# Kernel tuning notes

Hardware: AMD Instinct MI355X
Metric: run time of the kernel (lower is better)

Reference implementation:

```python
import jax, jax.numpy as jnp
import numpy as np

N = 100000   # nodes
E = 600000   # edges
D = 128      # d_model / hidden_dim
L = 4        # num_layers
V = 5000     # node vocab (in_size)
G = 128      # num graphs in batch
C = 10       # num_class
BN_EPS = 1e-5


def setup_inputs() -> dict:
    key = jax.random.key(0)
    ks = jax.random.split(key, 20)
    s = 0.05
    return {
        "x": jax.random.randint(ks[0], (N,), 0, V),
        "edge_index": jax.random.randint(ks[1], (2, E), 0, N),
        "edge_attr": jax.random.normal(ks[2], (E, 2), dtype=jnp.float32),
        "batch": jnp.sort(jax.random.randint(ks[3], (N,), 0, G)),
        # embedding table
        "emb": jax.random.normal(ks[4], (V, D), dtype=jnp.float32) * s,
        # per-layer GINEConv edge linear (edge_dim=2 -> D)
        "edge_w": jax.random.normal(ks[5], (L, 2, D), dtype=jnp.float32) * s,
        "edge_b": jnp.zeros((L, D), jnp.float32),
        # per-layer MLP: Linear -> BN -> ReLU -> Linear
        "w1": jax.random.normal(ks[6], (L, D, D), dtype=jnp.float32) * s,
        "b1": jnp.zeros((L, D), jnp.float32),
        "g1": jnp.ones((L, D), jnp.float32),
        "beta1": jnp.zeros((L, D), jnp.float32),
        "w2": jax.random.normal(ks[7], (L, D, D), dtype=jnp.float32) * s,
        "b2": jnp.zeros((L, D), jnp.float32),
        # per-layer outer BatchNorm (self.norms)
        "ng": jnp.ones((L, D), jnp.float32),
        "nb": jnp.zeros((L, D), jnp.float32),
        # classifier: Linear(D,D) -> ReLU -> Linear(D,C)
        "cw1": jax.random.normal(ks[8], (D, D), dtype=jnp.float32) * s,
        "cb1": jnp.zeros((D,), jnp.float32),
        "cw2": jax.random.normal(ks[9], (D, C), dtype=jnp.float32) * s,
        "cb2": jnp.zeros((C,), jnp.float32),
    }


def _bn(h, g, b):
    # training-mode BatchNorm1d over node axis, biased variance
    m = h.mean(0)
    v = h.var(0)
    return (h - m) * jax.lax.rsqrt(v + BN_EPS) * g + b


def reference(x, edge_index, edge_attr, batch, emb, edge_w, edge_b,
              w1, b1, g1, beta1, w2, b2, ng, nb, cw1, cb1, cw2, cb2):
    h = emb[x]                                    # [N, D]
    src, dst = edge_index[0], edge_index[1]
    for l in range(L):
        e = edge_attr @ edge_w[l] + edge_b[l]     # [E, D]
        msg = jax.nn.relu(h[src] + e)             # gather + add + relu
        agg = jax.ops.segment_sum(msg, dst, num_segments=N)  # scatter-sum
        z = h + agg                               # (1+eps)*x_i + aggr, eps=0
        z = jax.nn.relu(_bn(z @ w1[l] + b1[l], g1[l], beta1[l]))
        h = _bn(z @ w2[l] + b2[l], ng[l], nb[l])
        if l != L - 1:
            h = jax.nn.relu(h)
    sums = jax.ops.segment_sum(h, batch, num_segments=G)            # [G, D]
    counts = jax.ops.segment_sum(jnp.ones((N, 1), h.dtype), batch, num_segments=G)
    pooled = sums / jnp.maximum(counts, 1.0)      # global mean pool
    return jax.nn.relu(pooled @ cw1 + cb1) @ cw2 + cb2  # [G, C]
```

## Files before the change

kernel.cpp:

```cpp
#include <hip/hip_runtime.h>
#include <stdint.h>

#define N_NODES 100000
#define N_EDGES 600000
#define DMODEL  128
#define NLAYERS 4
#define NGRAPH  128
#define NCLASS  10
#define BN_EPS  1e-5f
#define NSLOT   32
#define STATSZ  (NSLOT * 2 * DMODEL)

typedef __bf16 bf16x8 __attribute__((ext_vector_type(8)));
typedef __bf16 bf16x4 __attribute__((ext_vector_type(4)));
typedef __bf16 bf16x2 __attribute__((ext_vector_type(2)));
typedef float  f32x4  __attribute__((ext_vector_type(4)));

__global__ void k_init(int* __restrict__ deg, float* __restrict__ statA,
                       float* __restrict__ statB, float* __restrict__ psum,
                       const float* __restrict__ w1, const float* __restrict__ w2,
                       __bf16* __restrict__ wt_hi, __bf16* __restrict__ wt_lo,
                       const int* __restrict__ batch, int* __restrict__ gstart) {
  int i = blockIdx.x * 256 + threadIdx.x;
  if (i < N_NODES) deg[i] = 0;
  if (i < NLAYERS * STATSZ) {
    statA[i] = 0.0f;
    statB[i] = 0.0f;
  }
  if (i < NGRAPH * DMODEL) psum[i] = 0.0f;
  {
    int mat = i >> 14;
    int rem = i & 16383;
    int n = rem >> 7;
    int k = rem & 127;
    int l = mat >> 1;
    int which = mat & 1;
    const float* w = which ? w2 : w1;
    float v = w[(size_t)l * DMODEL * DMODEL + (size_t)k * DMODEL + n];
    __bf16 hi = (__bf16)v;
    wt_hi[i] = hi;
    wt_lo[i] = (__bf16)(v - (float)hi);
  }
  if (i <= NGRAPH) {
    int lo = 0;
    int hi = N_NODES;
    while (lo < hi) {
      int mid = (lo + hi) >> 1;
      if (batch[mid] < i) lo = mid + 1; else hi = mid;
    }
    gstart[i] = lo;
  }
}

__global__ void k_embed(const int* __restrict__ x, const float* __restrict__ emb,
                        __bf16* __restrict__ h) {
  int idx = blockIdx.x * 256 + threadIdx.x;
  if (idx >= N_NODES * DMODEL / 8) return;
  int i = idx >> 4;
  int p = idx & 15;
  const float* src = emb + (size_t)x[i] * DMODEL + p * 8;
  float4 v0 = *(const float4*)(src);
  float4 v1 = *(const float4*)(src + 4);
  bf16x8 o;
  o[0] = (__bf16)v0.x; o[1] = (__bf16)v0.y; o[2] = (__bf16)v0.z; o[3] = (__bf16)v0.w;
  o[4] = (__bf16)v1.x; o[5] = (__bf16)v1.y; o[6] = (__bf16)v1.z; o[7] = (__bf16)v1.w;
  *(bf16x8*)(h + (size_t)i * DMODEL + p * 8) = o;
}

__global__ void k_hist(const int* __restrict__ dst, int* __restrict__ deg) {
  int e = blockIdx.x * 256 + threadIdx.x;
  if (e < N_EDGES) atomicAdd(&deg[dst[e]], 1);
}

__global__ void k_scan1(const int* __restrict__ deg, int* __restrict__ out,
                        int* __restrict__ bsum, int n) {
  __shared__ int lds[256];
  int t = threadIdx.x;
  int idx = blockIdx.x * 256 + t;
  int v = (idx < n) ? deg[idx] : 0;
  int val = v;
  lds[t] = val;
  for (int ofs = 1; ofs < 256; ofs <<= 1) {
    __syncthreads();
    int u = (t >= ofs) ? lds[t - ofs] : 0;
    __syncthreads();
    val += u;
    lds[t] = val;
  }
  if (idx < n) out[idx] = val - v;
  if (t == 255) bsum[blockIdx.x] = val;
}

__global__ void k_scan2(const int* __restrict__ bsum, int* __restrict__ bsumx, int nb) {
  __shared__ int lds[512];
  int t = threadIdx.x;
  int v = (t < nb) ? bsum[t] : 0;
  int val = v;
  lds[t] = val;
  for (int ofs = 1; ofs < 512; ofs <<= 1) {
    __syncthreads();
    int u = (t >= ofs) ? lds[t - ofs] : 0;
    __syncthreads();
    val += u;
    lds[t] = val;
  }
  if (t < nb) bsumx[t] = val - v;
}

__global__ void k_scan3(int* __restrict__ row_start, int* __restrict__ cursor,
                        const int* __restrict__ bsumx, int n, int total) {
  int idx = blockIdx.x * 256 + threadIdx.x;
  if (idx < n) {
    int v = row_start[idx] + bsumx[blockIdx.x];
    row_start[idx] = v;
    cursor[idx] = v;
  }
  if (idx == 0) row_start[n] = total;
}

__global__ void k_scatter(const int* __restrict__ ei, const float* __restrict__ ea,
                          int* __restrict__ cursor, int4* __restrict__ epack) {
  int e = blockIdx.x * 256 + threadIdx.x;
  if (e >= N_EDGES) return;
  int s = ei[e];
  int d = ei[N_EDGES + e];
  int pos = atomicAdd(&cursor[d], 1);
  int4 pk;
  pk.x = s;
  pk.y = __float_as_int(ea[2 * e]);
  pk.z = __float_as_int(ea[2 * e + 1]);
  pk.w = 0;
  epack[pos] = pk;
}

__global__ void __launch_bounds__(256) k_agg(
    const __bf16* __restrict__ h, const int* __restrict__ row_start,
    const int4* __restrict__ epack,
    const float* __restrict__ ew,
    const float* __restrict__ ebp,
    const float* __restrict__ statPrev,
    const float* __restrict__ gamma, const float* __restrict__ beta, int hasT,
    __bf16* __restrict__ z) {
  __shared__ float sld[DMODEL];
  __shared__ float tld[DMODEL];
  int tid = threadIdx.x;
  if (hasT) {
    if (tid < DMODEL) {
      float sum = 0.0f;
      float sq = 0.0f;
      for (int p = 0; p < NSLOT; ++p) {
        sum += statPrev[p * (2 * DMODEL) + tid];
        sq  += statPrev[p * (2 * DMODEL) + DMODEL + tid];
      }
      float mean = sum * (1.0f / N_NODES);
      float var = sq * (1.0f / N_NODES) - mean * mean;
      float inv = rsqrtf(var + BN_EPS);
      float s = gamma[tid] * inv;
      sld[tid] = s;
      tld[tid] = beta[tid] - mean * s;
    }
    __syncthreads();
  }

  int node = blockIdx.x * 8 + (tid >> 5);
  int ln = tid & 31;
  int d0 = ln * 4;

  float4 ew0 = *(const float4*)(ew + d0);
  float4 ew1 = *(const float4*)(ew + DMODEL + d0);
  float4 eb  = *(const float4*)(ebp + d0);
  float4 s4;
  float4 t4;
  if (hasT) {
    s4 = *(const float4*)(sld + d0);
    t4 = *(const float4*)(tld + d0);
  }

  bf16x4 hv = *(const bf16x4*)(h + (size_t)node * DMODEL + d0);
  float acc0, acc1, acc2, acc3;
  {
    float r0 = (float)hv[0];
    float r1 = (float)hv[1];
    float r2 = (float)hv[2];
    float r3 = (float)hv[3];
    if (hasT) {
      acc0 = fmaxf(s4.x * r0 + t4.x, 0.0f);
      acc1 = fmaxf(s4.y * r1 + t4.y, 0.0f);
      acc2 = fmaxf(s4.z * r2 + t4.z, 0.0f);
      acc3 = fmaxf(s4.w * r3 + t4.w, 0.0f);
    } else {
      acc0 = r0; acc1 = r1; acc2 = r2; acc3 = r3;
    }
  }

  int j0 = row_start[node];
  int j1 = row_start[node + 1];
  int j = j0;

#define AGG_ONE(E, V)                                                          \
  {                                                                            \
    float a0 = __int_as_float((E).y);                                          \
    float a1 = __int_as_float((E).z);                                          \
    float f0 = (float)(V)[0];                                                  \
    float f1 = (float)(V)[1];                                                  \
    float f2 = (float)(V)[2];                                                  \
    float f3 = (float)(V)[3];                                                  \
    if (hasT) {                                                                \
      f0 = fmaxf(s4.x * f0 + t4.x, 0.0f);                                      \
      f1 = fmaxf(s4.y * f1 + t4.y, 0.0f);                                      \
      f2 = fmaxf(s4.z * f2 + t4.z, 0.0f);                                      \
      f3 = fmaxf(s4.w * f3 + t4.w, 0.0f);                                      \
    }                                                                          \
    acc0 += fmaxf(f0 + a0 * ew0.x + a1 * ew1.x + eb.x, 0.0f);                  \
    acc1 += fmaxf(f1 + a0 * ew0.y + a1 * ew1.y + eb.y, 0.0f);                  \
    acc2 += fmaxf(f2 + a0 * ew0.z + a1 * ew1.z + eb.z, 0.0f);                  \
    acc3 += fmaxf(f3 + a0 * ew0.w + a1 * ew1.w + eb.w, 0.0f);                  \
  }

  for (; j + 4 <= j1; j += 4) {
    int4 e0 = epack[j];
    int4 e1 = epack[j + 1];
    int4 e2 = epack[j + 2];
    int4 e3 = epack[j + 3];
    bf16x4 v0 = *(const bf16x4*)(h + (size_t)e0.x * DMODEL + d0);
    bf16x4 v1 = *(const bf16x4*)(h + (size_t)e1.x * DMODEL + d0);
    bf16x4 v2 = *(const bf16x4*)(h + (size_t)e2.x * DMODEL + d0);
    bf16x4 v3 = *(const bf16x4*)(h + (size_t)e3.x * DMODEL + d0);
    AGG_ONE(e0, v0)
    AGG_ONE(e1, v1)
    AGG_ONE(e2, v2)
    AGG_ONE(e3, v3)
  }
  for (; j < j1; ++j) {
    int4 e0 = epack[j];
    bf16x4 v0 = *(const bf16x4*)(h + (size_t)e0.x * DMODEL + d0);
    AGG_ONE(e0, v0)
  }
#undef AGG_ONE

  bf16x4 o;
  o[0] = (__bf16)acc0;
  o[1] = (__bf16)acc1;
  o[2] = (__bf16)acc2;
  o[3] = (__bf16)acc3;
  *(bf16x4*)(z + (size_t)node * DMODEL + d0) = o;
}

__global__ void __launch_bounds__(256) k_gemm1(
    const __bf16* __restrict__ X,
    const __bf16* __restrict__ Whi, const __bf16* __restrict__ Wlo,
    const float* __restrict__ bias,
    __bf16* __restrict__ Y,
    float* __restrict__ statpart) {
  int tid = threadIdx.x;
  int wave = tid >> 6;
  int lane = tid & 63;
  int n16 = lane & 15;
  int quad = lane >> 4;

  bf16x8 bhi[2][4];
  bf16x8 blo[2][4];
#pragma unroll
  for (int ct = 0; ct < 2; ++ct) {
    int n = (wave * 2 + ct) * 16 + n16;
#pragma unroll
    for (int kk = 0; kk < 4; ++kk) {
      int k0 = kk * 32 + quad * 8;
      bhi[ct][kk] = *(const bf16x8*)(Whi + (size_t)n * DMODEL + k0);
      blo[ct][kk] = *(const bf16x8*)(Wlo + (size_t)n * DMODEL + k0);
    }
  }
  float bc[2];
  bc[0] = bias[(wave * 2 + 0) * 16 + n16];
  bc[1] = bias[(wave * 2 + 1) * 16 + n16];

  float ssum[2] = {0.0f, 0.0f};
  float ssq[2] = {0.0f, 0.0f};

  const int NCHUNK = N_NODES / 32;
  for (int c = blockIdx.x; c < NCHUNK; c += gridDim.x) {
    int row0 = c * 32;
    bf16x8 a[2][4];
#pragma unroll
    for (int t = 0; t < 2; ++t) {
      const __bf16* xr = X + (size_t)(row0 + t * 16 + n16) * DMODEL;
#pragma unroll
      for (int kk = 0; kk < 4; ++kk) {
        a[t][kk] = *(const bf16x8*)(xr + kk * 32 + quad * 8);
      }
    }

    f32x4 acc[2][2];
#pragma unroll
    for (int t = 0; t < 2; ++t)
#pragma unroll
      for (int ct = 0; ct < 2; ++ct)
#pragma unroll
        for (int r = 0; r < 4; ++r) acc[t][ct][r] = 0.0f;

#pragma unroll
    for (int kk = 0; kk < 4; ++kk) {
#pragma unroll
      for (int ct = 0; ct < 2; ++ct) {
#pragma unroll
        for (int t = 0; t < 2; ++t) {
          acc[t][ct] = __builtin_amdgcn_mfma_f32_16x16x32_bf16(a[t][kk], bhi[ct][kk], acc[t][ct], 0, 0, 0);
          acc[t][ct] = __builtin_amdgcn_mfma_f32_16x16x32_bf16(a[t][kk], blo[ct][kk], acc[t][ct], 0, 0, 0);
        }
      }
    }

#pragma unroll
    for (int t = 0; t < 2; ++t) {
#pragma unroll
      for (int ct = 0; ct < 2; ++ct) {
        int col = (wave * 2 + ct) * 16 + n16;
#pragma unroll
        for (int r = 0; r < 4; ++r) {
          int row = row0 + t * 16 + quad * 4 + r;
          float v = acc[t][ct][r] + bc[ct];
          Y[(size_t)row * DMODEL + col] = (__bf16)v;
          ssum[ct] += v;
          ssq[ct] += v * v;
        }
      }
    }
  }

  int slot = blockIdx.x & (NSLOT - 1);
#pragma unroll
  for (int ct = 0; ct < 2; ++ct) {
    int col = (wave * 2 + ct) * 16 + n16;
    float s = ssum[ct];
    float q = ssq[ct];
    s += __shfl_xor(s, 16);
    q += __shfl_xor(q, 16);
    s += __shfl_xor(s, 32);
    q += __shfl_xor(q, 32);
    if (quad == 0) {
      atomicAdd(&statpart[slot * (2 * DMODEL) + col], s);
      atomicAdd(&statpart[slot * (2 * DMODEL) + DMODEL + col], q);
    }
  }
}

__global__ void __launch_bounds__(256) k_gemm2(
    const __bf16* __restrict__ X,
    const __bf16* __restrict__ Whi, const __bf16* __restrict__ Wlo,
    const float* __restrict__ bias,
    const float* __restrict__ statA,
    const float* __restrict__ gamma, const float* __restrict__ beta,
    __bf16* __restrict__ Y,
    float* __restrict__ statpart) {
  __shared__ float sld[DMODEL];
  __shared__ float tld[DMODEL];
  int tid = threadIdx.x;

  if (tid < DMODEL) {
    float sum = 0.0f;
    float sq = 0.0f;
    for (int p = 0; p < NSLOT; ++p) {
      sum += statA[p * (2 * DMODEL) + tid];
      sq  += statA[p * (2 * DMODEL) + DMODEL + tid];
    }
    float mean = sum * (1.0f / N_NODES);
    float var = sq * (1.0f / N_NODES) - mean * mean;
    float inv = rsqrtf(var + BN_EPS);
    float s = gamma[tid] * inv;
    sld[tid] = s;
    tld[tid] = beta[tid] - mean * s;
  }
  __syncthreads();

  int wave = tid >> 6;
  int lane = tid & 63;
  int n16 = lane & 15;
  int quad = lane >> 4;

  bf16x8 bhi[2][4];
  bf16x8 blo[2][4];
#pragma unroll
  for (int ct = 0; ct < 2; ++ct) {
    int n = (wave * 2 + ct) * 16 + n16;
#pragma unroll
    for (int kk = 0; kk < 4; ++kk) {
      int k0 = kk * 32 + quad * 8;
      bhi[ct][kk] = *(const bf16x8*)(Whi + (size_t)n * DMODEL + k0);
      blo[ct][kk] = *(const bf16x8*)(Wlo + (size_t)n * DMODEL + k0);
    }
  }
  float bc[2];
  bc[0] = bias[(wave * 2 + 0) * 16 + n16];
  bc[1] = bias[(wave * 2 + 1) * 16 + n16];

  float ssum[2] = {0.0f, 0.0f};
  float ssq[2] = {0.0f, 0.0f};

  const int NCHUNK = N_NODES / 32;
  for (int c = blockIdx.x; c < NCHUNK; c += gridDim.x) {
    int row0 = c * 32;
    bf16x8 a[2][4];
#pragma unroll
    for (int t = 0; t < 2; ++t) {
      const __bf16* xr = X + (size_t)(row0 + t * 16 + n16) * DMODEL;
#pragma unroll
      for (int kk = 0; kk < 4; ++kk) {
        a[t][kk] = *(const bf16x8*)(xr + kk * 32 + quad * 8);
      }
    }
#pragma unroll
    for (int kk = 0; kk < 4; ++kk) {
      int k0 = kk * 32 + quad * 8;
      float4 s0 = *(const float4*)(sld + k0);
      float4 s1 = *(const float4*)(sld + k0 + 4);
      float4 t0 = *(const float4*)(tld + k0);
      float4 t1 = *(const float4*)(tld + k0 + 4);
      float sv[8];
      float tv[8];
      sv[0] = s0.x; sv[1] = s0.y; sv[2] = s0.z; sv[3] = s0.w;
      sv[4] = s1.x; sv[5] = s1.y; sv[6] = s1.z; sv[7] = s1.w;
      tv[0] = t0.x; tv[1] = t0.y; tv[2] = t0.z; tv[3] = t0.w;
      tv[4] = t1.x; tv[5] = t1.y; tv[6] = t1.z; tv[7] = t1.w;
#pragma unroll
      for (int t = 0; t < 2; ++t) {
#pragma unroll
        for (int jj = 0; jj < 8; ++jj) {
          float f = (float)a[t][kk][jj];
          a[t][kk][jj] = (__bf16)fmaxf(sv[jj] * f + tv[jj], 0.0f);
        }
      }
    }

    f32x4 acc[2][2];
#pragma unroll
    for (int t = 0; t < 2; ++t)
#pragma unroll
      for (int ct = 0; ct < 2; ++ct)
#pragma unroll
        for (int r = 0; r < 4; ++r) acc[t][ct][r] = 0.0f;

#pragma unroll
    for (int kk = 0; kk < 4; ++kk) {
#pragma unroll
      for (int ct = 0; ct < 2; ++ct) {
#pragma unroll
        for (int t = 0; t < 2; ++t) {
          acc[t][ct] = __builtin_amdgcn_mfma_f32_16x16x32_bf16(a[t][kk], bhi[ct][kk], acc[t][ct], 0, 0, 0);
          acc[t][ct] = __builtin_amdgcn_mfma_f32_16x16x32_bf16(a[t][kk], blo[ct][kk], acc[t][ct], 0, 0, 0);
        }
      }
    }

#pragma unroll
    for (int t = 0; t < 2; ++t) {
#pragma unroll
      for (int ct = 0; ct < 2; ++ct) {
        int col = (wave * 2 + ct) * 16 + n16;
#pragma unroll
        for (int r = 0; r < 4; ++r) {
          int row = row0 + t * 16 + quad * 4 + r;
          float v = acc[t][ct][r] + bc[ct];
          Y[(size_t)row * DMODEL + col] = (__bf16)v;
          ssum[ct] += v;
          ssq[ct] += v * v;
        }
      }
    }
  }

  int slot = blockIdx.x & (NSLOT - 1);
#pragma unroll
  for (int ct = 0; ct < 2; ++ct) {
    int col = (wave * 2 + ct) * 16 + n16;
    float s = ssum[ct];
    float q = ssq[ct];
    s += __shfl_xor(s, 16);
    q += __shfl_xor(q, 16);
    s += __shfl_xor(s, 32);
    q += __shfl_xor(q, 32);
    if (quad == 0) {
      atomicAdd(&statpart[slot * (2 * DMODEL) + col], s);
      atomicAdd(&statpart[slot * (2 * DMODEL) + DMODEL + col], q);
    }
  }
}

__global__ void k_pool(const __bf16* __restrict__ h, const int* __restrict__ gstart,
                       float* __restrict__ psum) {
  int g = blockIdx.x;
  int slice = blockIdx.y;
  int lane = threadIdx.x;
  int d0 = lane * 2;
  int i0 = gstart[g];
  int i1 = gstart[g + 1];
  float a0 = 0.0f;
  float a1 = 0.0f;
  for (int i = i0 + slice; i < i1; i += 8) {
    bf16x2 v = *(const bf16x2*)(h + (size_t)i * DMODEL + d0);
    a0 += (float)v[0];
    a1 += (float)v[1];
  }
  atomicAdd(&psum[g * DMODEL + d0], a0);
  atomicAdd(&psum[g * DMODEL + d0 + 1], a1);
}

__global__ void k_classifier(const float* __restrict__ psum, const int* __restrict__ gstart,
                             const float* __restrict__ statB,
                             const float* __restrict__ gamma, const float* __restrict__ beta,
                             const float* __restrict__ cw1, const float* __restrict__ cb1,
                             const float* __restrict__ cw2, const float* __restrict__ cb2,
                             float* __restrict__ out) {
  __shared__ float pl[DMODEL];
  __shared__ float hid[DMODEL];
  int g = blockIdx.x;
  int d = threadIdx.x;
  float sum = 0.0f;
  float sq = 0.0f;
  for (int p = 0; p < NSLOT; ++p) {
    sum += statB[p * (2 * DMODEL) + d];
    sq  += statB[p * (2 * DMODEL) + DMODEL + d];
  }
  float mean = sum * (1.0f / N_NODES);
  float var = sq * (1.0f / N_NODES) - mean * mean;
  float inv = rsqrtf(var + BN_EPS);
  float s2 = gamma[d] * inv;
  float t2 = beta[d] - mean * s2;

  int cnt = gstart[g + 1] - gstart[g];
  pl[d] = (cnt > 0) ? (s2 * (psum[g * DMODEL + d] / (float)cnt) + t2) : 0.0f;
  __syncthreads();
  float acc = cb1[d];
  for (int k = 0; k < DMODEL; ++k) acc += pl[k] * cw1[k * DMODEL + d];
  hid[d] = fmaxf(acc, 0.0f);
  __syncthreads();
  if (d < NCLASS) {
    float acc2 = cb2[d];
    for (int k = 0; k < DMODEL; ++k) acc2 += hid[k] * cw2[k * NCLASS + d];
    out[g * NCLASS + d] = acc2;
  }
}

extern "C" void kernel_launch(void* const* d_in, const int* in_sizes, int n_in,
                              void* d_out, int out_size, void* d_ws, size_t ws_size,
                              hipStream_t stream) {
  const int*   x      = (const int*)d_in[0];
  const int*   ei     = (const int*)d_in[1];
  const float* ea     = (const float*)d_in[2];
  const int*   batch  = (const int*)d_in[3];
  const float* emb    = (const float*)d_in[4];
  const float* edge_w = (const float*)d_in[5];
  const float* edge_b = (const float*)d_in[6];
  const float* w1     = (const float*)d_in[7];
  const float* b1     = (const float*)d_in[8];
  const float* g1     = (const float*)d_in[9];
  const float* beta1  = (const float*)d_in[10];
  const float* w2     = (const float*)d_in[11];
  const float* b2     = (const float*)d_in[12];
  const float* ng     = (const float*)d_in[13];
  const float* nb     = (const float*)d_in[14];
  const float* cw1    = (const float*)d_in[15];
  const float* cb1    = (const float*)d_in[16];
  const float* cw2    = (const float*)d_in[17];
  const float* cb2    = (const float*)d_in[18];

  char* ws = (char*)d_ws;
  size_t off = 0;
  auto alloc = [&](size_t bytes) -> void* {
    void* p = ws + off;
    off += (bytes + 255) & ~(size_t)255;
    return p;
  };

  __bf16* h_bf      = (__bf16*)alloc((size_t)N_NODES * DMODEL * sizeof(__bf16));
  __bf16* z_bf      = (__bf16*)alloc((size_t)N_NODES * DMODEL * sizeof(__bf16));
  __bf16* y1_bf     = (__bf16*)alloc((size_t)N_NODES * DMODEL * sizeof(__bf16));
  int*    row_start = (int*)alloc((N_NODES + 1) * sizeof(int));
  int*    cursor    = (int*)alloc(N_NODES * sizeof(int));
  int*    deg       = (int*)alloc(N_NODES * sizeof(int));
  int4*   epack     = (int4*)alloc((size_t)N_EDGES * sizeof(int4));
  __bf16* wt_hi     = (__bf16*)alloc((size_t)NLAYERS * 2 * DMODEL * DMODEL * sizeof(__bf16));
  __bf16* wt_lo     = (__bf16*)alloc((size_t)NLAYERS * 2 * DMODEL * DMODEL * sizeof(__bf16));
  float*  statA     = (float*)alloc((size_t)NLAYERS * STATSZ * sizeof(float));
  float*  statB     = (float*)alloc((size_t)NLAYERS * STATSZ * sizeof(float));
  int*    gstart    = (int*)alloc((NGRAPH + 1) * sizeof(int));
  float*  psum      = (float*)alloc((size_t)NGRAPH * DMODEL * sizeof(float));
  int*    bsum      = (int*)alloc(512 * sizeof(int));
  int*    bsumx     = (int*)alloc(512 * sizeof(int));

  auto statAL = [&](int l) { return statA + (size_t)l * STATSZ; };
  auto statBL = [&](int l) { return statB + (size_t)l * STATSZ; };

  const int nbScan = (N_NODES + 255) / 256;
  const int nbEdge = (N_EDGES + 255) / 256;
  const int nbEmb  = (N_NODES * DMODEL / 8 + 255) / 256;
  const int nbGemm = 782;
  const int nbAgg  = N_NODES / 8;

  k_init<<<512, 256, 0, stream>>>(deg, statA, statB, psum,
                                  w1, w2, wt_hi, wt_lo, batch, gstart);
  k_embed<<<nbEmb, 256, 0, stream>>>(x, emb, h_bf);
  k_hist<<<nbEdge, 256, 0, stream>>>(ei + N_EDGES, deg);
  k_scan1<<<nbScan, 256, 0, stream>>>(deg, row_start, bsum, N_NODES);
  k_scan2<<<1, 512, 0, stream>>>(bsum, bsumx, nbScan);
  k_scan3<<<nbScan, 256, 0, stream>>>(row_start, cursor, bsumx, N_NODES, N_EDGES);
  k_scatter<<<nbEdge, 256, 0, stream>>>(ei, ea, cursor, epack);

  for (int l = 0; l < NLAYERS; ++l) {
    const float* sPrev = (l > 0) ? statBL(l - 1) : (const float*)nullptr;
    const float* gPrev = (l > 0) ? (ng + (size_t)(l - 1) * DMODEL) : (const float*)nullptr;
    const float* bPrev = (l > 0) ? (nb + (size_t)(l - 1) * DMODEL) : (const float*)nullptr;
    k_agg<<<nbAgg, 256, 0, stream>>>(h_bf, row_start, epack,
                                     edge_w + (size_t)l * 2 * DMODEL,
                                     edge_b + (size_t)l * DMODEL,
                                     sPrev, gPrev, bPrev, (l > 0) ? 1 : 0, z_bf);
    k_gemm1<<<nbGemm, 256, 0, stream>>>(
        z_bf,
        wt_hi + (size_t)(l * 2 + 0) * DMODEL * DMODEL,
        wt_lo + (size_t)(l * 2 + 0) * DMODEL * DMODEL,
        b1 + (size_t)l * DMODEL,
        y1_bf, statAL(l));
    k_gemm2<<<nbGemm, 256, 0, stream>>>(
        y1_bf,
        wt_hi + (size_t)(l * 2 + 1) * DMODEL * DMODEL,
        wt_lo + (size_t)(l * 2 + 1) * DMODEL * DMODEL,
        b2 + (size_t)l * DMODEL,
        statAL(l), g1 + (size_t)l * DMODEL, beta1 + (size_t)l * DMODEL,
        h_bf, statBL(l));
  }

  dim3 poolGrid(NGRAPH, 8);
  k_pool<<<poolGrid, 64, 0, stream>>>(h_bf, gstart, psum);
  k_classifier<<<NGRAPH, DMODEL, 0, stream>>>(psum, gstart, statBL(NLAYERS - 1),
                                              ng + (size_t)(NLAYERS - 1) * DMODEL,
                                              nb + (size_t)(NLAYERS - 1) * DMODEL,
                                              cw1, cb1, cw2, cb2, (float*)d_out);
}
```

Before: 673.6 us.

## Fuse edge aggregation with first MLP GEMM via shared-memory tile

Merges the aggregation kernel and the first GEMM: each block aggregates 32 nodes into a padded LDS tile, then runs the MFMA GEMM with bias and BN statistics directly from that tile. This removes the z intermediate's global write and read-back and one kernel launch per layer. In exchange, the grid grows from a fixed persistent count to one block per 32 nodes, so every block reloads the weight fragments. Each half-wave now processes four nodes serially, and the GEMM waits at a barrier for the slowest gather.

```diff
diff --git a/kernel.cpp b/kernel.cpp
--- a/kernel.cpp
+++ b/kernel.cpp
@@ -10,6 +10,7 @@
 #define BN_EPS  1e-5f
 #define NSLOT   32
 #define STATSZ  (NSLOT * 2 * DMODEL)
+#define ZSTR    136
 
 typedef __bf16 bf16x8 __attribute__((ext_vector_type(8)));
 typedef __bf16 bf16x4 __attribute__((ext_vector_type(4)));
@@ -133,17 +134,22 @@
   epack[pos] = pk;
 }
 
-__global__ void __launch_bounds__(256) k_agg(
+__global__ void __launch_bounds__(256) k_aggemm(
     const __bf16* __restrict__ h, const int* __restrict__ row_start,
     const int4* __restrict__ epack,
     const float* __restrict__ ew,
     const float* __restrict__ ebp,
     const float* __restrict__ statPrev,
-    const float* __restrict__ gamma, const float* __restrict__ beta, int hasT,
-    __bf16* __restrict__ z) {
+    const float* __restrict__ gammaP, const float* __restrict__ betaP, int hasT,
+    const __bf16* __restrict__ Whi, const __bf16* __restrict__ Wlo,
+    const float* __restrict__ bias,
+    __bf16* __restrict__ Y,
+    float* __restrict__ statpart) {
+  __shared__ __align__(16) __bf16 zt[32 * ZSTR];
   __shared__ float sld[DMODEL];
   __shared__ float tld[DMODEL];
   int tid = threadIdx.x;
+
   if (hasT) {
     if (tid < DMODEL) {
       float sum = 0.0f;
@@ -155,14 +161,14 @@
       float mean = sum * (1.0f / N_NODES);
       float var = sq * (1.0f / N_NODES) - mean * mean;
       float inv = rsqrtf(var + BN_EPS);
-      float s = gamma[tid] * inv;
+      float s = gammaP[tid] * inv;
       sld[tid] = s;
-      tld[tid] = beta[tid] - mean * s;
+      tld[tid] = betaP[tid] - mean * s;
     }
     __syncthreads();
   }
 
-  int node = blockIdx.x * 8 + (tid >> 5);
+  int hw = tid >> 5;
   int ln = tid & 31;
   int d0 = ln * 4;
 
@@ -175,27 +181,6 @@
     s4 = *(const float4*)(sld + d0);
     t4 = *(const float4*)(tld + d0);
   }
-
-  bf16x4 hv = *(const bf16x4*)(h + (size_t)node * DMODEL + d0);
-  float acc0, acc1, acc2, acc3;
-  {
-    float r0 = (float)hv[0];
-    float r1 = (float)hv[1];
-    float r2 = (float)hv[2];
-    float r3 = (float)hv[3];
-    if (hasT) {
-      acc0 = fmaxf(s4.x * r0 + t4.x, 0.0f);
-      acc1 = fmaxf(s4.y * r1 + t4.y, 0.0f);
-      acc2 = fmaxf(s4.z * r2 + t4.z, 0.0f);
-      acc3 = fmaxf(s4.w * r3 + t4.w, 0.0f);
-    } else {
-      acc0 = r0; acc1 = r1; acc2 = r2; acc3 = r3;
-    }
-  }
-
-  int j0 = row_start[node];
-  int j1 = row_start[node + 1];
-  int j = j0;
 
 #define AGG_ONE(E, V)                                                          \
   {                                                                            \
@@ -217,42 +202,58 @@
     acc3 += fmaxf(f3 + a0 * ew0.w + a1 * ew1.w + eb.w, 0.0f);                  \
   }
 
-  for (; j + 4 <= j1; j += 4) {
-    int4 e0 = epack[j];
-    int4 e1 = epack[j + 1];
-    int4 e2 = epack[j + 2];
-    int4 e3 = epack[j + 3];
-    bf16x4 v0 = *(const bf16x4*)(h + (size_t)e0.x * DMODEL + d0);
-    bf16x4 v1 = *(const bf16x4*)(h + (size_t)e1.x * DMODEL + d0);
-    bf16x4 v2 = *(const bf16x4*)(h + (size_t)e2.x * DMODEL + d0);
-    bf16x4 v3 = *(const bf16x4*)(h + (size_t)e3.x * DMODEL + d0);
-    AGG_ONE(e0, v0)
-    AGG_ONE(e1, v1)
-    AGG_ONE(e2, v2)
-    AGG_ONE(e3, v3)
-  }
-  for (; j < j1; ++j) {
-    int4 e0 = epack[j];
-    bf16x4 v0 = *(const bf16x4*)(h + (size_t)e0.x * DMODEL + d0);
-    AGG_ONE(e0, v0)
+  for (int i = 0; i < 4; ++i) {
+    int nl = hw * 4 + i;
+    int node = blockIdx.x * 32 + nl;
+    bf16x4 hv = *(const bf16x4*)(h + (size_t)node * DMODEL + d0);
+    float acc0, acc1, acc2, acc3;
+    {
+      float r0 = (float)hv[0];
+      float r1 = (float)hv[1];
+      float r2 = (float)hv[2];
+      float r3 = (float)hv[3];
+      if (hasT) {
+        acc0 = fmaxf(s4.x * r0 + t4.x, 0.0f);
+        acc1 = fmaxf(s4.y * r1 + t4.y, 0.0f);
+        acc2 = fmaxf(s4.z * r2 + t4.z, 0.0f);
+        acc3 = fmaxf(s4.w * r3 + t4.w, 0.0f);
+      } else {
+        acc0 = r0; acc1 = r1; acc2 = r2; acc3 = r3;
+      }
+    }
+    int j0 = row_start[node];
+    int j1 = row_start[node + 1];
+    int j = j0;
+    for (; j + 4 <= j1; j += 4) {
+      int4 e0 = epack[j];
+      int4 e1 = epack[j + 1];
+      int4 e2 = epack[j + 2];
+      int4 e3 = epack[j + 3];
+      bf16x4 v0 = *(const bf16x4*)(h + (size_t)e0.x * DMODEL + d0);
+      bf16x4 v1 = *(const bf16x4*)(h + (size_t)e1.x * DMODEL + d0);
+      bf16x4 v2 = *(const bf16x4*)(h + (size_t)e2.x * DMODEL + d0);
+      bf16x4 v3 = *(const bf16x4*)(h + (size_t)e3.x * DMODEL + d0);
+      AGG_ONE(e0, v0)
+      AGG_ONE(e1, v1)
+      AGG_ONE(e2, v2)
+      AGG_ONE(e3, v3)
+    }
+    for (; j < j1; ++j) {
+      int4 e0 = epack[j];
+      bf16x4 v0 = *(const bf16x4*)(h + (size_t)e0.x * DMODEL + d0);
+      AGG_ONE(e0, v0)
+    }
+    bf16x4 o;
+    o[0] = (__bf16)acc0;
+    o[1] = (__bf16)acc1;
+    o[2] = (__bf16)acc2;
+    o[3] = (__bf16)acc3;
+    *(bf16x4*)(zt + nl * ZSTR + d0) = o;
   }
 #undef AGG_ONE
 
-  bf16x4 o;
-  o[0] = (__bf16)acc0;
-  o[1] = (__bf16)acc1;
-  o[2] = (__bf16)acc2;
-  o[3] = (__bf16)acc3;
-  *(bf16x4*)(z + (size_t)node * DMODEL + d0) = o;
-}
-
-__global__ void __launch_bounds__(256) k_gemm1(
-    const __bf16* __restrict__ X,
-    const __bf16* __restrict__ Whi, const __bf16* __restrict__ Wlo,
-    const float* __restrict__ bias,
-    __bf16* __restrict__ Y,
-    float* __restrict__ statpart) {
-  int tid = threadIdx.x;
+  __syncthreads();
+
   int wave = tid >> 6;
   int lane = tid & 63;
   int n16 = lane & 15;
@@ -274,55 +275,51 @@
   bc[0] = bias[(wave * 2 + 0) * 16 + n16];
   bc[1] = bias[(wave * 2 + 1) * 16 + n16];
 
+  bf16x8 a[2][4];
+#pragma unroll
+  for (int t = 0; t < 2; ++t) {
+    const __bf16* zr = zt + (t * 16 + n16) * ZSTR;
+#pragma unroll
+    for (int kk = 0; kk < 4; ++kk) {
+      a[t][kk] = *(const bf16x8*)(zr + kk * 32 + quad * 8);
+    }
+  }
+
+  f32x4 acc[2][2];
+#pragma unroll
+  for (int t = 0; t < 2; ++t)
+#pragma unroll
+    for (int ct = 0; ct < 2; ++ct)
+#pragma unroll
+      for (int r = 0; r < 4; ++r) acc[t][ct][r] = 0.0f;
+
+#pragma unroll
+  for (int kk = 0; kk < 4; ++kk) {
+#pragma unroll
+    for (int ct = 0; ct < 2; ++ct) {
+#pragma unroll
+      for (int t = 0; t < 2; ++t) {
+        acc[t][ct] = __builtin_amdgcn_mfma_f32_16x16x32_bf16(a[t][kk], bhi[ct][kk], acc[t][ct], 0, 0, 0);
+        acc[t][ct] = __builtin_amdgcn_mfma_f32_16x16x32_bf16(a[t][kk], blo[ct][kk], acc[t][ct], 0, 0, 0);
+      }
+    }
+  }
+
+  int row0 = blockIdx.x * 32;
   float ssum[2] = {0.0f, 0.0f};
   float ssq[2] = {0.0f, 0.0f};
-
-  const int NCHUNK = N_NODES / 32;
-  for (int c = blockIdx.x; c < NCHUNK; c += gridDim.x) {
-    int row0 = c * 32;
-    bf16x8 a[2][4];
-#pragma unroll
-    for (int t = 0; t < 2; ++t) {
-      const __bf16* xr = X + (size_t)(row0 + t * 16 + n16) * DMODEL;
-#pragma unroll
-      for (int kk = 0; kk < 4; ++kk) {
-        a[t][kk] = *(const bf16x8*)(xr + kk * 32 + quad * 8);
-      }
-    }
-
-    f32x4 acc[2][2];
-#pragma unroll
-    for (int t = 0; t < 2; ++t)
-#pragma unroll
-      for (int ct = 0; ct < 2; ++ct)
-#pragma unroll
-        for (int r = 0; r < 4; ++r) acc[t][ct][r] = 0.0f;
-
-#pragma unroll
-    for (int kk = 0; kk < 4; ++kk) {
-#pragma unroll
-      for (int ct = 0; ct < 2; ++ct) {
-#pragma unroll
-        for (int t = 0; t < 2; ++t) {
-          acc[t][ct] = __builtin_amdgcn_mfma_f32_16x16x32_bf16(a[t][kk], bhi[ct][kk], acc[t][ct], 0, 0, 0);
-          acc[t][ct] = __builtin_amdgcn_mfma_f32_16x16x32_bf16(a[t][kk], blo[ct][kk], acc[t][ct], 0, 0, 0);
-        }
-      }
-    }
-
-#pragma unroll
-    for (int t = 0; t < 2; ++t) {
-#pragma unroll
-      for (int ct = 0; ct < 2; ++ct) {
-        int col = (wave * 2 + ct) * 16 + n16;
-#pragma unroll
-        for (int r = 0; r < 4; ++r) {
-          int row = row0 + t * 16 + quad * 4 + r;
-          float v = acc[t][ct][r] + bc[ct];
-          Y[(size_t)row * DMODEL + col] = (__bf16)v;
-          ssum[ct] += v;
-          ssq[ct] += v * v;
-        }
+#pragma unroll
+  for (int t = 0; t < 2; ++t) {
+#pragma unroll
+    for (int ct = 0; ct < 2; ++ct) {
+      int col = (wave * 2 + ct) * 16 + n16;
+#pragma unroll
+      for (int r = 0; r < 4; ++r) {
+        int row = row0 + t * 16 + quad * 4 + r;
+        float v = acc[t][ct][r] + bc[ct];
+        Y[(size_t)row * DMODEL + col] = (__bf16)v;
+        ssum[ct] += v;
+        ssq[ct] += v * v;
       }
     }
   }
@@ -572,7 +569,6 @@
   };
 
   __bf16* h_bf      = (__bf16*)alloc((size_t)N_NODES * DMODEL * sizeof(__bf16));
-  __bf16* z_bf      = (__bf16*)alloc((size_t)N_NODES * DMODEL * sizeof(__bf16));
   __bf16* y1_bf     = (__bf16*)alloc((size_t)N_NODES * DMODEL * sizeof(__bf16));
   int*    row_start = (int*)alloc((N_NODES + 1) * sizeof(int));
   int*    cursor    = (int*)alloc(N_NODES * sizeof(int));
@@ -594,7 +590,7 @@
   const int nbEdge = (N_EDGES + 255) / 256;
   const int nbEmb  = (N_NODES * DMODEL / 8 + 255) / 256;
   const int nbGemm = 782;
-  const int nbAgg  = N_NODES / 8;
+  const int nbFuse = N_NODES / 32;
 
   k_init<<<512, 256, 0, stream>>>(deg, statA, statB, psum,
                                   w1, w2, wt_hi, wt_lo, batch, gstart);
@@ -609,12 +605,11 @@
     const float* sPrev = (l > 0) ? statBL(l - 1) : (const float*)nullptr;
     const float* gPrev = (l > 0) ? (ng + (size_t)(l - 1) * DMODEL) : (const float*)nullptr;
     const float* bPrev = (l > 0) ? (nb + (size_t)(l - 1) * DMODEL) : (const float*)nullptr;
-    k_agg<<<nbAgg, 256, 0, stream>>>(h_bf, row_start, epack,
-                                     edge_w + (size_t)l * 2 * DMODEL,
-                                     edge_b + (size_t)l * DMODEL,
-                                     sPrev, gPrev, bPrev, (l > 0) ? 1 : 0, z_bf);
-    k_gemm1<<<nbGemm, 256, 0, stream>>>(
-        z_bf,
+    k_aggemm<<<nbFuse, 256, 0, stream>>>(
+        h_bf, row_start, epack,
+        edge_w + (size_t)l * 2 * DMODEL,
+        edge_b + (size_t)l * DMODEL,
+        sPrev, gPrev, bPrev, (l > 0) ? 1 : 0,
         wt_hi + (size_t)(l * 2 + 0) * DMODEL * DMODEL,
         wt_lo + (size_t)(l * 2 + 0) * DMODEL * DMODEL,
         b1 + (size_t)l * DMODEL,
```

After: 664.0 us. About the same (-1.4%).
